# Performance work log

Hardware: AMD Instinct MI355X
Metric: run time of the kernel (lower is better)

The kernel has to match this reference:

```python
import jax, jax.numpy as jnp
import numpy as np

B, S, H, L = 32, 2048, 256, 2


def setup_inputs() -> dict:
    key = jax.random.key(0)
    k = jax.random.split(key, 5)
    scale = 1.0 / np.sqrt(H)  # torch-style uniform-ish init scale, use scaled normal
    return {
        "inputs": jax.random.normal(k[0], (B, S, H), dtype=jnp.float32),
        "h0": jnp.zeros((L, B, H), dtype=jnp.float32),
        "W_ih": jax.random.normal(k[1], (L, H, H), dtype=jnp.float32) * scale,
        "W_hh": jax.random.normal(k[2], (L, H, H), dtype=jnp.float32) * scale,
        "b_ih": jax.random.normal(k[3], (L, H), dtype=jnp.float32) * scale,
        "b_hh": jax.random.normal(k[4], (L, H), dtype=jnp.float32) * scale,
    }


def reference(inputs, h0, W_ih, W_hh, b_ih, b_hh):
    """Multi-layer unidirectional Elman RNN (tanh), batch_first, delay=1.

    Matches BaseRNN/RNNLayer: per timestep out, h_new = cell(x_t, h);
    with a vanilla cell out == h_new = tanh(x W_ih^T + b_ih + h W_hh^T + b_hh).
    Returns (outputs [B,S,H] of last layer, final hidden [L,B,H]).
    """
    x = inputs
    finals = []
    n_layers = W_ih.shape[0]
    for l in range(n_layers):  # small fixed loop over layers
        # hoist the input projection out of the recurrence: [B,S,H]
        xp = jnp.einsum("bsi,hi->bsh", x, W_ih[l]) + b_ih[l]
        Whh_l = W_hh[l]
        bhh_l = b_hh[l]

        def step(h, xt):
            h_new = jnp.tanh(xt + h @ Whh_l.T + bhh_l)
            return h_new, h_new

        h_last, ys = jax.lax.scan(step, h0[l], jnp.swapaxes(xp, 0, 1))  # ys: [S,B,H]
        x = jnp.swapaxes(ys, 0, 1)  # [B,S,H]
        finals.append(h_last)
    return x, jnp.stack(finals, axis=0)
```

## Files before the change

### kernel.cpp

```cpp
#include <hip/hip_runtime.h>
#include <cstddef>

#define Bn 32
#define Sn 2048
#define Hn 256
#define Ln 2
#define CHUNK 32
#define NCHUNK (Sn / CHUNK)
#define PACE 2

#define PSTR 10
#define PBUF (Hn * PSTR)

#define FPAD 32
#define NFL (5 * Bn)

typedef float f32x2 __attribute__((ext_vector_type(2)));

__device__ unsigned g_flags[NFL * FPAD];

__global__ void zero_flags_k() {
  int i = threadIdx.x;
  if (i < NFL)
    __hip_atomic_store(&g_flags[i * FPAD], 0u, __ATOMIC_RELAXED,
                       __HIP_MEMORY_SCOPE_AGENT);
}

__device__ __forceinline__ float tanh_fast(float x) {
  float e = __expf(2.0f * x);
  return 1.0f - 2.0f / (e + 1.0f);
}

__device__ __forceinline__ float ldg_dev(const float* p) {
  return __hip_atomic_load(p, __ATOMIC_RELAXED, __HIP_MEMORY_SCOPE_AGENT);
}
__device__ __forceinline__ void stg_dev(float* p, float v) {
  __hip_atomic_store(p, v, __ATOMIC_RELAXED, __HIP_MEMORY_SCOPE_AGENT);
}

__device__ __forceinline__ void poll_ge_n(unsigned* base, int n, unsigned tgt) {
  for (int q = 0; q < n; ++q) {
    unsigned* f = base + (size_t)q * Bn * FPAD;
    while (__hip_atomic_load(f, __ATOMIC_RELAXED, __HIP_MEMORY_SCOPE_AGENT) < tgt)
      __builtin_amdgcn_s_sleep(32);
  }
}

__device__ __forceinline__ void publish(unsigned* f, unsigned val, int t) {
  asm volatile("s_waitcnt vmcnt(0)" ::: "memory");
  __syncthreads();
  if (t == 0)
    __hip_atomic_store(f, val, __ATOMIC_RELAXED, __HIP_MEMORY_SCOPE_AGENT);
}

template <bool XP_SC1, bool Y_SC1>
__device__ void rec_body(const float* __restrict__ xp_b,
                         const float* __restrict__ Whh,
                         const float* __restrict__ bhh,
                         const float* __restrict__ h0_b,
                         float* __restrict__ y_b,
                         float* __restrict__ hfin_b,
                         unsigned* wbase, int nw, unsigned* pub,
                         float* part, float* hbuf) {
  const int t = threadIdx.x;
  const int lane = t & 63;
  const int w = t >> 6;
  const int ocol = 32 * w + (lane & 31);

  f32x2 Wreg[4][16];
#pragma unroll
  for (int r = 0; r < 4; ++r)
#pragma unroll
    for (int q = 0; q < 8; ++q) {
      float4 v = *(const float4*)&Whh[(size_t)(lane + 64 * r) * Hn + 32 * w + 4 * q];
      Wreg[r][2 * q + 0] = f32x2{v.x, v.y};
      Wreg[r][2 * q + 1] = f32x2{v.z, v.w};
    }
#pragma unroll
  for (int r = 0; r < 4; ++r)
#pragma unroll
    for (int c = 0; c < 16; ++c)
      asm("" : "+v"(Wreg[r][c]));

  const int pw0 = PSTR * lane + (w ^ ((lane >> 3) & 3));
  const float bias = bhh[ocol];

  f32x2 hv[16];
#pragma unroll
  for (int j = 0; j < 8; ++j) {
    float4 v = *(const float4*)&h0_b[32 * w + 4 * j];
    hv[2 * j + 0] = f32x2{v.x, v.y};
    hv[2 * j + 1] = f32x2{v.z, v.w};
  }

  for (int c = 0; c < NCHUNK; ++c) {
    if (t == 0) poll_ge_n(wbase, nw, c + 1);
    __syncthreads();

    const int s0 = c * CHUNK;
    float xp_cur = ldg_dev(&xp_b[(size_t)s0 * Hn + ocol]);
    float xp_n1  = ldg_dev(&xp_b[(size_t)(s0 + 1) * Hn + ocol]);

    for (int ss = 0; ss < CHUNK; ++ss) {
      const int s = s0 + ss;
      float xp_n2 = 0.0f;
      if (s + 2 < Sn)
        xp_n2 = XP_SC1 ? ldg_dev(&xp_b[(size_t)(s + 2) * Hn + ocol])
                       : xp_b[(size_t)(s + 2) * Hn + ocol];

      f32x2 acc0 = {0.f, 0.f}, acc1 = {0.f, 0.f};
      f32x2 acc2 = {0.f, 0.f}, acc3 = {0.f, 0.f};
#pragma unroll
      for (int cc = 0; cc < 16; ++cc) {
        asm("v_pk_fma_f32 %0, %1, %2, %0" : "+v"(acc0) : "v"(Wreg[0][cc]), "v"(hv[cc]));
        asm("v_pk_fma_f32 %0, %1, %2, %0" : "+v"(acc1) : "v"(Wreg[1][cc]), "v"(hv[cc]));
        asm("v_pk_fma_f32 %0, %1, %2, %0" : "+v"(acc2) : "v"(Wreg[2][cc]), "v"(hv[cc]));
        asm("v_pk_fma_f32 %0, %1, %2, %0" : "+v"(acc3) : "v"(Wreg[3][cc]), "v"(hv[cc]));
      }
      float* pbuf = &part[(s & 1) * PBUF];
      pbuf[pw0       ] = acc0.x + acc0.y;
      pbuf[pw0 +  640] = acc1.x + acc1.y;
      pbuf[pw0 + 1280] = acc2.x + acc2.y;
      pbuf[pw0 + 1920] = acc3.x + acc3.y;

      asm volatile("s_waitcnt lgkmcnt(0)" ::: "memory");
      __builtin_amdgcn_s_barrier();
      __builtin_amdgcn_sched_barrier(0);

      const f32x2* prow = (const f32x2*)&pbuf[PSTR * ocol];
      f32x2 p0 = prow[0], p1 = prow[1], p2 = prow[2], p3 = prow[3];
      f32x2 q01 = p0 + p1;
      f32x2 q23 = p2 + p3;
      f32x2 qq = q01 + q23;
      float hn = tanh_fast((qq.x + qq.y) + xp_cur + bias);
      if (lane < 32) {
        hbuf[ocol] = hn;
        if (Y_SC1) stg_dev(&y_b[(size_t)s * Hn + ocol], hn);
        else       y_b[(size_t)s * Hn + ocol] = hn;
      }
      xp_cur = xp_n1;
      xp_n1 = xp_n2;

      __builtin_amdgcn_wave_barrier();
#pragma unroll
      for (int j = 0; j < 8; ++j) {
        float4 v = *(const float4*)&hbuf[32 * w + 4 * j];
        hv[2 * j + 0] = f32x2{v.x, v.y};
        hv[2 * j + 1] = f32x2{v.z, v.w};
      }
    }

    if (pub) publish(pub, (unsigned)(c + 1), t);
  }

  if (lane < 32) hfin_b[ocol] = hbuf[ocol];
}

__device__ void proj_body(const float* __restrict__ Ab,
                          const float* __restrict__ W,
                          const float* __restrict__ bias,
                          float* __restrict__ Cb,
                          unsigned* waitf, unsigned* pace, unsigned* pub,
                          int nt0, int nt1,
                          float* smem) {
  const int t = threadIdx.x;
  const int tx = t & 15;
  const int ty = t >> 4;
  float (*As)[34] = (float(*)[34])smem;
  float (*Bs)[68] = (float(*)[68])(smem + 64 * 34);

  for (int c = 0; c < NCHUNK; ++c) {
    if (waitf || pace) {
      if (t == 0) {
        if (waitf) poll_ge_n(waitf, 1, c + 1);
        if (pace && c > PACE) poll_ge_n(pace, 1, (unsigned)(c - PACE));
      }
      __syncthreads();
    }
    const float* A = Ab + (size_t)(c * CHUNK) * Hn;
    float* C = Cb + (size_t)(c * CHUNK) * Hn;

    for (int nt = nt0; nt < nt1; ++nt) {
      const int n0 = nt * 64;
      float acc[4] = {0.f, 0.f, 0.f, 0.f};
      for (int kc = 0; kc < Hn; kc += 64) {
        {
          int mm = t >> 4;
          int kk = (t & 15) << 2;
          float4 av = *(const float4*)&A[(size_t)mm * Hn + kc + kk];
          As[kk + 0][mm] = av.x; As[kk + 1][mm] = av.y;
          As[kk + 2][mm] = av.z; As[kk + 3][mm] = av.w;
        }
#pragma unroll
        for (int r = 0; r < 2; ++r) {
          int idx = t + 512 * r;
          int mm = idx >> 4;
          int kk = (idx & 15) << 2;
          float4 wv = *(const float4*)&W[(size_t)(n0 + mm) * Hn + kc + kk];
          Bs[kk + 0][mm] = wv.x; Bs[kk + 1][mm] = wv.y;
          Bs[kk + 2][mm] = wv.z; Bs[kk + 3][mm] = wv.w;
        }
        __syncthreads();
#pragma unroll
        for (int k = 0; k < 64; ++k) {
          float a = As[k][ty];
          float4 bv = *(const float4*)&Bs[k][tx << 2];
          acc[0] += a * bv.x; acc[1] += a * bv.y;
          acc[2] += a * bv.z; acc[3] += a * bv.w;
        }
        __syncthreads();
      }
      float4 bb = *(const float4*)&bias[n0 + (tx << 2)];
      float* cp = &C[(size_t)ty * Hn + n0 + (tx << 2)];
      stg_dev(cp + 0, acc[0] + bb.x);
      stg_dev(cp + 1, acc[1] + bb.y);
      stg_dev(cp + 2, acc[2] + bb.z);
      stg_dev(cp + 3, acc[3] + bb.w);
    }

    publish(pub, (unsigned)(c + 1), t);
  }
}

__global__ __launch_bounds__(512)
__attribute__((amdgpu_waves_per_eu(2, 2)))
void fused(
    const float* __restrict__ x, const float* __restrict__ h0,
    const float* __restrict__ Wih, const float* __restrict__ Whh,
    const float* __restrict__ bih, const float* __restrict__ bhh,
    float* __restrict__ yout, float* __restrict__ fin,
    float* __restrict__ xpws) {
  __shared__ float smem[2 * 64 * 68];
  const int bid = blockIdx.x;

  if (bid < 32) {
    const int b = bid;
    rec_body<false, true>(xpws + (size_t)b * Sn * Hn, Whh, bhh,
                          h0 + (size_t)b * Hn,
                          yout + (size_t)b * Sn * Hn, fin + (size_t)b * Hn,
                          &g_flags[(0 * Bn + b) * FPAD], 2,
                          &g_flags[(2 * Bn + b) * FPAD],
                          smem, smem + 2 * PBUF);
  } else if (bid < 64) {
    const int b = bid - 32;
    rec_body<true, false>(xpws + (size_t)b * Sn * Hn, Whh + Hn * Hn, bhh + Hn,
                          h0 + (size_t)Bn * Hn + (size_t)b * Hn,
                          yout + (size_t)b * Sn * Hn,
                          fin + (size_t)Bn * Hn + (size_t)b * Hn,
                          &g_flags[(3 * Bn + b) * FPAD], 2, nullptr,
                          smem, smem + 2 * PBUF);
  } else if (bid < 128) {
    const int q = bid - 64;
    const int b = q & 31, j = q >> 5;
    proj_body(x + (size_t)b * Sn * Hn, Wih, bih, xpws + (size_t)b * Sn * Hn,
              nullptr, &g_flags[(2 * Bn + b) * FPAD],
              &g_flags[((0 + j) * Bn + b) * FPAD],
              2 * j, 2 * j + 2, smem);
  } else {
    const int q = bid - 128;
    const int b = q & 31, j = q >> 5;
    proj_body(yout + (size_t)b * Sn * Hn, Wih + Hn * Hn, bih + Hn,
              xpws + (size_t)b * Sn * Hn,
              &g_flags[(2 * Bn + b) * FPAD], nullptr,
              &g_flags[((3 + j) * Bn + b) * FPAD],
              2 * j, 2 * j + 2, smem);
  }
}

extern "C" void kernel_launch(void* const* d_in, const int* in_sizes, int n_in,
                              void* d_out, int out_size, void* d_ws, size_t ws_size,
                              hipStream_t stream) {
  const float* x   = (const float*)d_in[0];
  const float* h0  = (const float*)d_in[1];
  const float* Wih = (const float*)d_in[2];
  const float* Whh = (const float*)d_in[3];
  const float* bih = (const float*)d_in[4];
  const float* bhh = (const float*)d_in[5];

  float* out = (float*)d_out;
  float* yout = out;
  float* fin  = out + (size_t)Bn * Sn * Hn;
  float* xpws = (float*)d_ws;

  zero_flags_k<<<1, 256, 0, stream>>>();
  fused<<<192, 512, 0, stream>>>(x, h0, Wih, Whh, bih, bhh, yout, fin, xpws);
}
```

Baseline: 1.759 ms.

## Stage layer outputs in LDS, batch stores, and use one projection block per batch

The recurrence blocks now write each chunk's hidden states into a shared-memory buffer and flush them to global memory at chunk end with vectorized dwordx4 sc1 stores, replacing per-step scalar atomic stores. Projection work moves from two blocks per batch (each covering half the output columns) to one block per batch covering all four column tiles, which cuts the grid from 192 to 128 blocks and halves the flags polled per chunk. Projection outputs are also written with vector sc1 stores. In exchange, each projection block does twice the work serially, the chunk-end flush adds latency before publishing, and the larger shared buffer raises LDS use per block.

After: 2.646 ms. 1.5x slower.

```diff
diff --git a/kernel.cpp b/kernel.cpp
--- a/kernel.cpp
+++ b/kernel.cpp
@@ -13,9 +13,10 @@
 #define PBUF (Hn * PSTR)
 
 #define FPAD 32
-#define NFL (5 * Bn)
+#define NFL (3 * Bn)
 
 typedef float f32x2 __attribute__((ext_vector_type(2)));
+typedef float f32x4 __attribute__((ext_vector_type(4)));
 
 __device__ unsigned g_flags[NFL * FPAD];
 
@@ -34,16 +35,14 @@
 __device__ __forceinline__ float ldg_dev(const float* p) {
   return __hip_atomic_load(p, __ATOMIC_RELAXED, __HIP_MEMORY_SCOPE_AGENT);
 }
-__device__ __forceinline__ void stg_dev(float* p, float v) {
-  __hip_atomic_store(p, v, __ATOMIC_RELAXED, __HIP_MEMORY_SCOPE_AGENT);
-}
-
-__device__ __forceinline__ void poll_ge_n(unsigned* base, int n, unsigned tgt) {
-  for (int q = 0; q < n; ++q) {
-    unsigned* f = base + (size_t)q * Bn * FPAD;
-    while (__hip_atomic_load(f, __ATOMIC_RELAXED, __HIP_MEMORY_SCOPE_AGENT) < tgt)
-      __builtin_amdgcn_s_sleep(32);
-  }
+__device__ __forceinline__ void stg_dev4(float* p, f32x4 v) {
+  asm volatile("global_store_dwordx4 %0, %1, off sc1"
+               :: "v"(p), "v"(v) : "memory");
+}
+
+__device__ __forceinline__ void poll_ge(unsigned* f, unsigned tgt) {
+  while (__hip_atomic_load(f, __ATOMIC_RELAXED, __HIP_MEMORY_SCOPE_AGENT) < tgt)
+    __builtin_amdgcn_s_sleep(32);
 }
 
 __device__ __forceinline__ void publish(unsigned* f, unsigned val, int t) {
@@ -60,8 +59,8 @@
                          const float* __restrict__ h0_b,
                          float* __restrict__ y_b,
                          float* __restrict__ hfin_b,
-                         unsigned* wbase, int nw, unsigned* pub,
-                         float* part, float* hbuf) {
+                         unsigned* waitf, unsigned* pub,
+                         float* part, float* hbuf, float* ybuf) {
   const int t = threadIdx.x;
   const int lane = t & 63;
   const int w = t >> 6;
@@ -94,7 +93,7 @@
   }
 
   for (int c = 0; c < NCHUNK; ++c) {
-    if (t == 0) poll_ge_n(wbase, nw, c + 1);
+    if (t == 0) poll_ge(waitf, c + 1);
     __syncthreads();
 
     const int s0 = c * CHUNK;
@@ -135,8 +134,7 @@
       float hn = tanh_fast((qq.x + qq.y) + xp_cur + bias);
       if (lane < 32) {
         hbuf[ocol] = hn;
-        if (Y_SC1) stg_dev(&y_b[(size_t)s * Hn + ocol], hn);
-        else       y_b[(size_t)s * Hn + ocol] = hn;
+        ybuf[ss * Hn + ocol] = hn;
       }
       xp_cur = xp_n1;
       xp_n1 = xp_n2;
@@ -148,6 +146,18 @@
         hv[2 * j + 0] = f32x2{v.x, v.y};
         hv[2 * j + 1] = f32x2{v.z, v.w};
       }
+    }
+
+    __syncthreads();
+#pragma unroll
+    for (int i = 0; i < 4; ++i) {
+      int idx = t + 512 * i;
+      int row = idx >> 6;
+      int c4 = (idx & 63) << 2;
+      f32x4 v = *(const f32x4*)&ybuf[row * Hn + c4];
+      float* gp = &y_b[(size_t)(s0 + row) * Hn + c4];
+      if (Y_SC1) stg_dev4(gp, v);
+      else       *(f32x4*)gp = v;
     }
 
     if (pub) publish(pub, (unsigned)(c + 1), t);
@@ -161,7 +171,6 @@
                           const float* __restrict__ bias,
                           float* __restrict__ Cb,
                           unsigned* waitf, unsigned* pace, unsigned* pub,
-                          int nt0, int nt1,
                           float* smem) {
   const int t = threadIdx.x;
   const int tx = t & 15;
@@ -170,17 +179,16 @@
   float (*Bs)[68] = (float(*)[68])(smem + 64 * 34);
 
   for (int c = 0; c < NCHUNK; ++c) {
-    if (waitf || pace) {
-      if (t == 0) {
-        if (waitf) poll_ge_n(waitf, 1, c + 1);
-        if (pace && c > PACE) poll_ge_n(pace, 1, (unsigned)(c - PACE));
-      }
-      __syncthreads();
-    }
+    if (t == 0) {
+      if (waitf) poll_ge(waitf, c + 1);
+      if (pace && c > PACE) poll_ge(pace, (unsigned)(c - PACE));
+    }
+    __syncthreads();
+
     const float* A = Ab + (size_t)(c * CHUNK) * Hn;
     float* C = Cb + (size_t)(c * CHUNK) * Hn;
 
-    for (int nt = nt0; nt < nt1; ++nt) {
+    for (int nt = 0; nt < 4; ++nt) {
       const int n0 = nt * 64;
       float acc[4] = {0.f, 0.f, 0.f, 0.f};
       for (int kc = 0; kc < Hn; kc += 64) {
@@ -211,11 +219,10 @@
         __syncthreads();
       }
       float4 bb = *(const float4*)&bias[n0 + (tx << 2)];
-      float* cp = &C[(size_t)ty * Hn + n0 + (tx << 2)];
-      stg_dev(cp + 0, acc[0] + bb.x);
-      stg_dev(cp + 1, acc[1] + bb.y);
-      stg_dev(cp + 2, acc[2] + bb.z);
-      stg_dev(cp + 3, acc[3] + bb.w);
+      f32x4 ov;
+      ov.x = acc[0] + bb.x; ov.y = acc[1] + bb.y;
+      ov.z = acc[2] + bb.z; ov.w = acc[3] + bb.w;
+      stg_dev4(&C[(size_t)ty * Hn + n0 + (tx << 2)], ov);
     }
 
     publish(pub, (unsigned)(c + 1), t);
@@ -230,7 +237,7 @@
     const float* __restrict__ bih, const float* __restrict__ bhh,
     float* __restrict__ yout, float* __restrict__ fin,
     float* __restrict__ xpws) {
-  __shared__ float smem[2 * 64 * 68];
+  __shared__ float smem[2 * PBUF + Hn + CHUNK * Hn];
   const int bid = blockIdx.x;
 
   if (bid < 32) {
@@ -238,32 +245,28 @@
     rec_body<false, true>(xpws + (size_t)b * Sn * Hn, Whh, bhh,
                           h0 + (size_t)b * Hn,
                           yout + (size_t)b * Sn * Hn, fin + (size_t)b * Hn,
-                          &g_flags[(0 * Bn + b) * FPAD], 2,
-                          &g_flags[(2 * Bn + b) * FPAD],
-                          smem, smem + 2 * PBUF);
+                          &g_flags[(0 * Bn + b) * FPAD],
+                          &g_flags[(1 * Bn + b) * FPAD],
+                          smem, smem + 2 * PBUF, smem + 2 * PBUF + Hn);
   } else if (bid < 64) {
     const int b = bid - 32;
     rec_body<true, false>(xpws + (size_t)b * Sn * Hn, Whh + Hn * Hn, bhh + Hn,
                           h0 + (size_t)Bn * Hn + (size_t)b * Hn,
                           yout + (size_t)b * Sn * Hn,
                           fin + (size_t)Bn * Hn + (size_t)b * Hn,
-                          &g_flags[(3 * Bn + b) * FPAD], 2, nullptr,
-                          smem, smem + 2 * PBUF);
-  } else if (bid < 128) {
-    const int q = bid - 64;
-    const int b = q & 31, j = q >> 5;
+                          &g_flags[(2 * Bn + b) * FPAD], nullptr,
+                          smem, smem + 2 * PBUF, smem + 2 * PBUF + Hn);
+  } else if (bid < 96) {
+    const int b = bid - 64;
     proj_body(x + (size_t)b * Sn * Hn, Wih, bih, xpws + (size_t)b * Sn * Hn,
-              nullptr, &g_flags[(2 * Bn + b) * FPAD],
-              &g_flags[((0 + j) * Bn + b) * FPAD],
-              2 * j, 2 * j + 2, smem);
+              nullptr, &g_flags[(1 * Bn + b) * FPAD],
+              &g_flags[(0 * Bn + b) * FPAD], smem);
   } else {
-    const int q = bid - 128;
-    const int b = q & 31, j = q >> 5;
+    const int b = bid - 96;
     proj_body(yout + (size_t)b * Sn * Hn, Wih + Hn * Hn, bih + Hn,
               xpws + (size_t)b * Sn * Hn,
-              &g_flags[(2 * Bn + b) * FPAD], nullptr,
-              &g_flags[((3 + j) * Bn + b) * FPAD],
-              2 * j, 2 * j + 2, smem);
+              &g_flags[(1 * Bn + b) * FPAD], nullptr,
+              &g_flags[(2 * Bn + b) * FPAD], smem);
   }
 }
 
@@ -282,6 +285,6 @@
   float* fin  = out + (size_t)Bn * Sn * Hn;
   float* xpws = (float*)d_ws;
 
-  zero_flags_k<<<1, 256, 0, stream>>>();
-  fused<<<192, 512, 0, stream>>>(x, h0, Wih, Whh, bih, bhh, yout, fin, xpws);
-}
+  zero_flags_k<<<1, 128, 0, stream>>>();
+  fused<<<128, 512, 0, stream>>>(x, h0, Wih, Whh, bih, bhh, yout, fin, xpws);
+}
```
